# Kernel optimization log

Measured on AMD Instinct MI355X. Metric: run time of the kernel, lower is better.

Reference implementation:

```python
import jax, jax.numpy as jnp
import numpy as np

TEMPERATURE = 30.0
LN_EPS = 1e-5

B, CIN, COUT, S, HID, K = 64, 256, 512, 4096, 64, 4


def setup_inputs() -> dict:
    key = jax.random.key(0)
    ks = jax.random.split(key, 4)
    x = jax.random.normal(ks[0], (B, CIN, S), dtype=jnp.float32)
    w1 = jax.random.normal(ks[1], (HID, CIN), dtype=jnp.float32) * (1.0 / np.sqrt(CIN))
    w2 = jax.random.normal(ks[2], (K, HID), dtype=jnp.float32) * (1.0 / np.sqrt(HID))
    b2 = jnp.zeros((K,), dtype=jnp.float32)
    conv_w = jax.random.normal(ks[3], (K, COUT, CIN), dtype=jnp.float32) * (1.0 / np.sqrt(CIN))
    conv_b = jnp.zeros((K, COUT), dtype=jnp.float32)
    gamma = jnp.ones((S,), dtype=jnp.float32)
    beta = jnp.zeros((S,), dtype=jnp.float32)
    return {"x": x, "w1": w1, "w2": w2, "b2": b2, "conv_w": conv_w,
            "conv_b": conv_b, "gamma": gamma, "beta": beta}


def reference(x, w1, w2, b2, conv_w, conv_b, gamma, beta):
    # --- attention over K kernel experts (global avg pool -> FC -> ReLU -> FC -> softmax/T) ---
    pooled = x.mean(axis=-1)                               # [B, Cin]
    h = jax.nn.relu(pooled @ w1.T)                         # [B, H]
    logits = h @ w2.T + b2                                 # [B, K]
    att = jax.nn.softmax(logits / TEMPERATURE, axis=-1)    # [B, K]
    # --- per-sample mixed 1x1 conv weights (grouped-conv trick == batched matmul) ---
    Wb = jnp.einsum('bk,koi->boi', att, conv_w)            # [B, Cout, Cin]
    bb = att @ conv_b                                      # [B, Cout]
    y = jnp.einsum('boi,bis->bos', Wb, x) + bb[:, :, None]  # [B, Cout, S]
    # --- LayerNorm over time axis (Samples) ---
    mu = y.mean(axis=-1, keepdims=True)
    var = y.var(axis=-1, keepdims=True)
    y = (y - mu) * jax.lax.rsqrt(var + LN_EPS) * gamma + beta
    # --- GELU (torch default: exact erf); dropout is identity in eval mode ---
    return jax.nn.gelu(y, approximate=False)
```

## Files before the change

### kernel.cpp

```cpp
#include <hip/hip_runtime.h>
#include <hip/hip_bf16.h>

#define B_   64
#define CIN  256
#define COUT 512
#define S_   4096
#define HID  64
#define KEXP 4

typedef float f32x4 __attribute__((ext_vector_type(4)));
typedef short bf16x8 __attribute__((ext_vector_type(8)));

static __device__ __forceinline__ unsigned short f2bf(float f) {
    union { float f; unsigned u; } c; c.f = f;
    unsigned r = c.u + 0x7FFFu + ((c.u >> 16) & 1u);
    return (unsigned short)(r >> 16);
}
static __device__ __forceinline__ float bf2f(unsigned short u) {
    union { unsigned u; float f; } c; c.u = ((unsigned)u) << 16;
    return c.f;
}

static __device__ __forceinline__ void gl16(const unsigned short* g, unsigned short* l) {
    __builtin_amdgcn_global_load_lds(
        (const __attribute__((address_space(1))) void*)g,
        (__attribute__((address_space(3))) void*)l,
        16, 0, 0);
}

#define GSTR 68
__global__ __launch_bounds__(512, 2) void k_gram_part(const float* __restrict__ x,
                                                      unsigned short* __restrict__ part,
                                                      float* __restrict__ ppart,
                                                      unsigned short* __restrict__ xF) {
    __shared__ unsigned short lds[256 * GSTR];
    int bid = blockIdx.x;
    int b = bid & 63, sc = bid >> 6;
    int t = threadIdx.x, lane = t & 63, wv = t >> 6;
    int wr = wv >> 1, wc = wv & 1;
    const float* xb = x + (size_t)b * CIN * S_;
    unsigned short* xFb = xF + (size_t)b * S_ * CIN;

    f32x4 acc[4][8] = {};
    float psum[8] = {0.f, 0.f, 0.f, 0.f, 0.f, 0.f, 0.f, 0.f};

    for (int step = 0; step < 16; ++step) {
        int s0 = sc * 1024 + step * 64;
        __syncthreads();
#pragma unroll
        for (int p = 0; p < 8; ++p) {
            int i = t + p * 512;
            int row = i >> 4, f4 = i & 15;
            float4 v = *(const float4*)(xb + (size_t)row * S_ + s0 + f4 * 4);
            psum[p] += v.x + v.y + v.z + v.w;
            unsigned short u[4] = {f2bf(v.x), f2bf(v.y), f2bf(v.z), f2bf(v.w)};
            *(uint2*)&lds[row * GSTR + f4 * 4] = *(const uint2*)u;
        }
        __syncthreads();
        {
#pragma unroll
            for (int it = 0; it < 4; ++it) {
                int slot = t + it * 512;
                int chunk = slot >> 6;
                int st_l = chunk >> 3, kb = chunk & 7;
                int l = slot & 63;
                unsigned short tmp[8];
#pragma unroll
                for (int j = 0; j < 8; ++j)
                    tmp[j] = lds[(kb * 32 + (l >> 4) * 8 + j) * GSTR + st_l * 16 + (l & 15)];
                *(uint4*)(xFb + ((size_t)((s0 >> 4) + st_l) * 8 + kb) * 512 + l * 8) = *(const uint4*)tmp;
            }
        }
#pragma unroll
        for (int kk = 0; kk < 2; ++kk) {
            bf16x8 bfr[8];
#pragma unroll
            for (int nf = 0; nf < 8; ++nf)
                bfr[nf] = *(const bf16x8*)&lds[(wc * 128 + nf * 16 + (lane & 15)) * GSTR + kk * 32 + (lane >> 4) * 8];
#pragma unroll
            for (int mfi = 0; mfi < 4; ++mfi) {
                bf16x8 afr = *(const bf16x8*)&lds[(wr * 64 + mfi * 16 + (lane & 15)) * GSTR + kk * 32 + (lane >> 4) * 8];
#pragma unroll
                for (int nf = 0; nf < 8; ++nf)
                    acc[mfi][nf] = __builtin_amdgcn_mfma_f32_16x16x32_bf16(afr, bfr[nf], acc[mfi][nf], 0, 0, 0);
            }
        }
    }
#pragma unroll
    for (int p = 0; p < 8; ++p) {
        float s = psum[p];
        s += __shfl_xor(s, 1); s += __shfl_xor(s, 2);
        s += __shfl_xor(s, 4); s += __shfl_xor(s, 8);
        if ((t & 15) == 0) ppart[((size_t)sc * 64 + b) * 256 + ((t + p * 512) >> 4)] = s;
    }
    unsigned short* pb = part + ((size_t)sc * 64 + b) * 65536;
#pragma unroll
    for (int mfi = 0; mfi < 4; ++mfi) {
#pragma unroll
        for (int r = 0; r < 4; ++r) {
            int row = wr * 64 + mfi * 16 + (lane >> 4) * 4 + r;
#pragma unroll
            for (int nf = 0; nf < 8; ++nf)
                pb[row * 256 + wc * 128 + nf * 16 + (lane & 15)] = f2bf(acc[mfi][nf][r]);
        }
    }
}

__global__ __launch_bounds__(256) void k_gred(const unsigned short* __restrict__ part,
                                              const float* __restrict__ ppart,
                                              unsigned short* __restrict__ ghat,
                                              float* __restrict__ pooled) {
    int b = blockIdx.x, t = threadIdx.x;
    const size_t bo = (size_t)b * 65536;
    const size_t scs = (size_t)64 * 65536;
    const float inv = 1.f / S_;
    for (int it = 0; it < 32; ++it) {
        size_t i = bo + (size_t)(it * 256 + t) * 8;
        union { uint4 v; unsigned short s[8]; } a0, a1, a2, a3, o;
        a0.v = *(const uint4*)(part + i);
        a1.v = *(const uint4*)(part + scs + i);
        a2.v = *(const uint4*)(part + 2 * scs + i);
        a3.v = *(const uint4*)(part + 3 * scs + i);
#pragma unroll
        for (int j = 0; j < 8; ++j)
            o.s[j] = f2bf((bf2f(a0.s[j]) + bf2f(a1.s[j]) + bf2f(a2.s[j]) + bf2f(a3.s[j])) * inv);
        *(uint4*)&ghat[i] = o.v;
    }
    float p = ppart[(size_t)b * 256 + t] + ppart[(size_t)(64 + b) * 256 + t]
            + ppart[(size_t)(128 + b) * 256 + t] + ppart[(size_t)(192 + b) * 256 + t];
    pooled[b * 256 + t] = p * inv;
}

__global__ __launch_bounds__(64) void k_att(const float* __restrict__ pooled,
                                            const float* __restrict__ w1,
                                            const float* __restrict__ w2,
                                            const float* __restrict__ b2,
                                            float* __restrict__ att_out) {
    int b = blockIdx.x, t = threadIdx.x;
    __shared__ float pl[CIN];
    __shared__ float hl[HID];
    __shared__ float satt[KEXP];
    for (int j = t; j < CIN; j += 64) pl[j] = pooled[b * CIN + j];
    __syncthreads();
    float acc = 0.f;
    const float* w1r = w1 + t * CIN;
#pragma unroll 4
    for (int c = 0; c < CIN; c += 4) {
        float4 w = *(const float4*)(w1r + c);
        acc += w.x * pl[c] + w.y * pl[c + 1] + w.z * pl[c + 2] + w.w * pl[c + 3];
    }
    hl[t] = fmaxf(acc, 0.f);
    __syncthreads();
    if (t < KEXP) {
        float a = 0.f;
        for (int j = 0; j < HID; ++j) a += hl[j] * w2[t * HID + j];
        satt[t] = (a + b2[t]) * (1.0f / 30.0f);
    }
    __syncthreads();
    if (t == 0) {
        float m = fmaxf(fmaxf(satt[0], satt[1]), fmaxf(satt[2], satt[3]));
        float e0 = expf(satt[0] - m), e1 = expf(satt[1] - m);
        float e2 = expf(satt[2] - m), e3 = expf(satt[3] - m);
        float inv = 1.f / (e0 + e1 + e2 + e3);
        att_out[b * KEXP + 0] = e0 * inv;
        att_out[b * KEXP + 1] = e1 * inv;
        att_out[b * KEXP + 2] = e2 * inv;
        att_out[b * KEXP + 3] = e3 * inv;
    }
}

__global__ __launch_bounds__(256) void k_wb(const float* __restrict__ conv_w,
                                            const float* __restrict__ att,
                                            unsigned short* __restrict__ wb) {
    int bid = blockIdx.x;
    int b = bid >> 5, o0 = (bid & 31) * 16;
    int t = threadIdx.x;
    int o = o0 + (t >> 4);
    int i0 = (t & 15) * 16;
    float ak[KEXP];
#pragma unroll
    for (int k = 0; k < KEXP; ++k) ak[k] = att[b * KEXP + k];
    float acc[16];
#pragma unroll
    for (int j = 0; j < 16; ++j) acc[j] = 0.f;
#pragma unroll
    for (int k = 0; k < KEXP; ++k) {
        const float* src = conv_w + ((size_t)(k * COUT + o)) * CIN + i0;
#pragma unroll
        for (int j4 = 0; j4 < 4; ++j4) {
            float4 v = *(const float4*)(src + j4 * 4);
            acc[j4 * 4 + 0] += ak[k] * v.x;
            acc[j4 * 4 + 1] += ak[k] * v.y;
            acc[j4 * 4 + 2] += ak[k] * v.z;
            acc[j4 * 4 + 3] += ak[k] * v.w;
        }
    }
    unsigned short us[16];
#pragma unroll
    for (int j = 0; j < 16; ++j) us[j] = f2bf(acc[j]);
    unsigned short* dst = wb + (size_t)(b * COUT + o) * CIN + i0;
    *(uint4*)(dst) = *(const uint4*)(us);
    *(uint4*)(dst + 8) = *(const uint4*)(us + 8);
}

#define ASTR 264

__global__ __launch_bounds__(256, 2) void k_z(const unsigned short* __restrict__ wb,
                                              const unsigned short* __restrict__ ghat,
                                              float* __restrict__ zout) {
    __shared__ unsigned short lds_a[128 * ASTR];
    int bid = blockIdx.x;
    int b = bid & 63;
    int tile = bid >> 6;
    int m0 = (tile & 3) * 128, n0 = (tile >> 2) * 128;
    int t = threadIdx.x;
    {
        int row = t >> 1, half = t & 1;
        const unsigned short* src = wb + (size_t)(b * COUT + m0 + row) * CIN + half * 128;
        unsigned short* dstrow = &lds_a[row * ASTR + half * 128];
#pragma unroll
        for (int j = 0; j < 16; ++j)
            *(uint4*)(dstrow + j * 8) = *(const uint4*)(src + j * 8);
    }
    __syncthreads();

    int lane = t & 63;
    int wid = t >> 6;
    int arow = lane & 15;
    int kq = lane >> 4;
    int col0 = n0 + wid * 32 + (lane & 15);
    int col1 = col0 + 16;
    const unsigned short* gb = ghat + (size_t)b * 256 * 256;

    f32x4 acc[8][2] = {};
#pragma unroll
    for (int kk = 0; kk < 8; ++kk) {
        bf16x8 b0 = *(const bf16x8*)(gb + (size_t)col0 * 256 + kk * 32 + kq * 8);
        bf16x8 b1 = *(const bf16x8*)(gb + (size_t)col1 * 256 + kk * 32 + kq * 8);
#pragma unroll
        for (int mf = 0; mf < 8; ++mf) {
            int row = mf * 16 + arow;
            bf16x8 a = *(const bf16x8*)&lds_a[row * ASTR + kk * 32 + kq * 8];
            acc[mf][0] = __builtin_amdgcn_mfma_f32_16x16x32_bf16(a, b0, acc[mf][0], 0, 0, 0);
            acc[mf][1] = __builtin_amdgcn_mfma_f32_16x16x32_bf16(a, b1, acc[mf][1], 0, 0, 0);
        }
    }
#pragma unroll
    for (int mf = 0; mf < 8; ++mf) {
#pragma unroll
        for (int r = 0; r < 4; ++r) {
            int row = m0 + mf * 16 + (lane >> 4) * 4 + r;
            size_t rb = ((size_t)b * COUT + row) * 256;
#pragma unroll
            for (int nf = 0; nf < 2; ++nf) {
                int col = n0 + wid * 32 + nf * 16 + (lane & 15);
                zout[rb + col] = acc[mf][nf][r];
            }
        }
    }
}

__global__ __launch_bounds__(256) void k_v(const float* __restrict__ z,
                                           const unsigned short* __restrict__ wb,
                                           const float* __restrict__ pooled,
                                           float* __restrict__ mu,
                                           float* __restrict__ rstd) {
    int gid = blockIdx.x * 4 + (threadIdx.x >> 6);
    int lane = threadIdx.x & 63;
    int b = gid >> 9;
    const float* zr = z + (size_t)gid * 256;
    const unsigned short* wr = wb + (size_t)gid * 256;

    float4 zv = *(const float4*)(zr + lane * 4);
    ushort4 wu = *(const ushort4*)(wr + lane * 4);
    float w0 = bf2f(wu.x), w1 = bf2f(wu.y), w2 = bf2f(wu.z), w3 = bf2f(wu.w);
    float4 pv = *(const float4*)(pooled + b * CIN + lane * 4);

    float v = zv.x * w0 + zv.y * w1 + zv.z * w2 + zv.w * w3;
    float m = pv.x * w0 + pv.y * w1 + pv.z * w2 + pv.w * w3;
#pragma unroll
    for (int off = 1; off < 64; off <<= 1) {
        v += __shfl_xor(v, off);
        m += __shfl_xor(m, off);
    }
    if (lane == 0) {
        float var = v - m * m;
        mu[gid] = m;
        rstd[gid] = rsqrtf(var + 1e-5f);
    }
}

static __device__ __forceinline__ float gelu_t(float z) {
    float d = -1.5957691216f * z * (1.f + 0.044715f * z * z);
    return z * __builtin_amdgcn_rcpf(1.f + __expf(d));
}

#define EPW 66
__global__ __launch_bounds__(512) void k_main14(const unsigned short* __restrict__ xF,
                                                const unsigned short* __restrict__ wb,
                                                const float* __restrict__ mu,
                                                const float* __restrict__ rstd,
                                                const float* __restrict__ gamma,
                                                const float* __restrict__ beta,
                                                float* __restrict__ out) {
    __shared__ unsigned short ring[3][8192];
    __shared__ float eps[8][32 * EPW];
    __shared__ float gb_lds[2048];
    __shared__ float be_lds[2048];

    int bid = blockIdx.x;
    int xcd = bid & 7;
    int local = bid >> 3;
    int rh = local & 1;
    int sq = (local >> 1) & 1;
    int bq = local >> 2;
    int b = xcd + 8 * bq;

    int t = threadIdx.x, lane = t & 63, w = t >> 6;
    int lm = lane & 15, lk = lane >> 4;
    int row0 = rh * 256 + w * 32;
    int colbase = sq * 2048;

    {
        float4 g4 = *(const float4*)(gamma + colbase + t * 4);
        float4 b4 = *(const float4*)(beta + colbase + t * 4);
        *(float4*)&gb_lds[t * 4] = g4;
        *(float4*)&be_lds[t * 4] = b4;
    }

    bf16x8 A[2][8];
    const unsigned short* wbb = wb + (size_t)(b * COUT + row0 + lm) * CIN + lk * 8;
#pragma unroll
    for (int rf = 0; rf < 2; ++rf)
#pragma unroll
        for (int kk = 0; kk < 8; ++kk)
            A[rf][kk] = *(const bf16x8*)(wbb + (size_t)(rf * 16) * CIN + kk * 32);

    int r0 = lane >> 3;
    int c4 = (lane & 7) * 4;
    float muf[4], rsf[4];
#pragma unroll
    for (int j = 0; j < 4; ++j) {
        int row = b * COUT + row0 + r0 + 8 * j;
        muf[j] = mu[row];
        rsf[j] = rstd[row];
    }
    float* outb = out + (size_t)(b * COUT + row0) * S_ + colbase;
    float* epw = &eps[w][0];

    const unsigned short* xFq = xF + (size_t)b * S_ * CIN + (size_t)sq * 524288;

#define STAGE(st_, slot_)                                                          \
    {                                                                              \
        gl16(xFq + (size_t)((st_) * 16 + 2 * w) * 512 + lane * 8,                  \
             &ring[slot_][(2 * w) * 512]);                                         \
        gl16(xFq + (size_t)((st_) * 16 + 2 * w + 1) * 512 + lane * 8,              \
             &ring[slot_][(2 * w + 1) * 512]);                                     \
    }

    STAGE(0, 0)
    STAGE(1, 1)
    __syncthreads();

    for (int st = 0; st < 64; ++st) {
        if (st + 2 < 64) {
            int sp = st + 2, slot = sp - (sp / 3) * 3;
            STAGE(sp, slot)
        }

        const unsigned short* sl = &ring[st - (st / 3) * 3][0];
        f32x4 acc[2][2] = {};
#pragma unroll
        for (int cf = 0; cf < 2; ++cf) {
            bf16x8 Bf[8];
#pragma unroll
            for (int kb = 0; kb < 8; ++kb)
                Bf[kb] = *(const bf16x8*)(sl + (cf * 8 + kb) * 512 + lane * 8);
#pragma unroll
            for (int kb = 0; kb < 8; ++kb) {
                acc[0][cf] = __builtin_amdgcn_mfma_f32_16x16x32_bf16(A[0][kb], Bf[kb], acc[0][cf], 0, 0, 0);
                acc[1][cf] = __builtin_amdgcn_mfma_f32_16x16x32_bf16(A[1][kb], Bf[kb], acc[1][cf], 0, 0, 0);
            }
        }

#pragma unroll
        for (int cf = 0; cf < 2; ++cf)
#pragma unroll
            for (int rf = 0; rf < 2; ++rf)
#pragma unroll
                for (int rr = 0; rr < 4; ++rr)
                    epw[(rf * 16 + lk * 4 + rr) * EPW + (st & 1) * 32 + cf * 16 + lm] =
                        acc[rf][cf][rr];

        if (st & 1) {
            int fg = st >> 1;
#pragma unroll
            for (int j = 0; j < 4; ++j) {
                int rloc = r0 + 8 * j;
#pragma unroll
                for (int seg = 0; seg < 2; ++seg) {
                    int cl = seg * 32 + c4;
                    float2 lo = *(const float2*)&epw[rloc * EPW + cl];
                    float2 hi = *(const float2*)&epw[rloc * EPW + cl + 2];
                    float4 g4 = *(const float4*)&gb_lds[fg * 64 + cl];
                    float4 b4 = *(const float4*)&be_lds[fg * 64 + cl];
                    float4 o;
                    o.x = gelu_t((lo.x - muf[j]) * rsf[j] * g4.x + b4.x);
                    o.y = gelu_t((lo.y - muf[j]) * rsf[j] * g4.y + b4.y);
                    o.z = gelu_t((hi.x - muf[j]) * rsf[j] * g4.z + b4.z);
                    o.w = gelu_t((hi.y - muf[j]) * rsf[j] * g4.w + b4.w);
                    *(float4*)(outb + (size_t)rloc * S_ + fg * 64 + cl) = o;
                }
            }
        }
        __syncthreads();
    }
#undef STAGE
}

extern "C" void kernel_launch(void* const* d_in, const int* in_sizes, int n_in,
                              void* d_out, int out_size, void* d_ws, size_t ws_size,
                              hipStream_t stream) {
    const float* x      = (const float*)d_in[0];
    const float* w1     = (const float*)d_in[1];
    const float* w2     = (const float*)d_in[2];
    const float* b2     = (const float*)d_in[3];
    const float* conv_w = (const float*)d_in[4];
    const float* gamma  = (const float*)d_in[6];
    const float* beta   = (const float*)d_in[7];
    float* out = (float*)d_out;

    float* pooled = (float*)d_ws;
    float* att    = (float*)((char*)d_ws + 65536);
    unsigned short* wb   = (unsigned short*)((char*)d_ws + 262144);
    unsigned short* ghat = (unsigned short*)((char*)d_ws + 17039360);
    float* mu   = (float*)((char*)d_ws + 25427968);
    float* rstd = (float*)((char*)d_ws + 25559040);
    float* ppart = (float*)((char*)d_ws + 25690112);
    unsigned short* xF = (unsigned short*)((char*)d_ws + 33554432);

    unsigned short* part = (unsigned short*)out;
    float* zbuf = (float*)((char*)d_out + 67108864);

    k_gram_part<<<256, 512, 0, stream>>>(x, part, ppart, xF);
    k_gred<<<B_, 256, 0, stream>>>(part, ppart, ghat, pooled);
    k_att<<<B_, 64, 0, stream>>>(pooled, w1, w2, b2, att);
    k_wb<<<B_ * 32, 256, 0, stream>>>(conv_w, att, wb);
    k_z<<<512, 256, 0, stream>>>(wb, ghat, zbuf);
    k_v<<<B_ * COUT / 4, 256, 0, stream>>>(zbuf, wb, pooled, mu, rstd);
    k_main14<<<256, 512, 0, stream>>>(xF, wb, mu, rstd, gamma, beta, out);
}
```

Measured before the change: 438.1 us.

## Halve per-block column span and deepen LDS ring to raise occupancy

The main fused GEMM+LayerNorm+GELU kernel now splits the time axis into four quarters instead of two, launching 512 blocks instead of 256. Each stage loads 16 columns per warp instead of 32 through a 4-deep ring instead of a 3-deep one, which shrinks LDS use. Launch bounds now request 4 blocks per CU, aiming for more resident waves and better latency hiding. The cost is twice as many blocks reloading the same A weights and mu/rstd, plus smaller MFMA batches and more barriers per unit of work.

```diff
diff --git a/kernel.cpp b/kernel.cpp
--- a/kernel.cpp
+++ b/kernel.cpp
@@ -295,37 +295,37 @@
     return z * __builtin_amdgcn_rcpf(1.f + __expf(d));
 }
 
-#define EPW 66
-__global__ __launch_bounds__(512) void k_main14(const unsigned short* __restrict__ xF,
-                                                const unsigned short* __restrict__ wb,
-                                                const float* __restrict__ mu,
-                                                const float* __restrict__ rstd,
-                                                const float* __restrict__ gamma,
-                                                const float* __restrict__ beta,
-                                                float* __restrict__ out) {
-    __shared__ unsigned short ring[3][8192];
+#define EPW 36
+__global__ __launch_bounds__(512, 4) void k_main15(const unsigned short* __restrict__ xF,
+                                                   const unsigned short* __restrict__ wb,
+                                                   const float* __restrict__ mu,
+                                                   const float* __restrict__ rstd,
+                                                   const float* __restrict__ gamma,
+                                                   const float* __restrict__ beta,
+                                                   float* __restrict__ out) {
+    __shared__ unsigned short ring[4][4096];
     __shared__ float eps[8][32 * EPW];
-    __shared__ float gb_lds[2048];
-    __shared__ float be_lds[2048];
+    __shared__ float gb_lds[1024];
+    __shared__ float be_lds[1024];
 
     int bid = blockIdx.x;
     int xcd = bid & 7;
     int local = bid >> 3;
     int rh = local & 1;
-    int sq = (local >> 1) & 1;
-    int bq = local >> 2;
+    int sq = (local >> 1) & 3;
+    int bq = local >> 3;
     int b = xcd + 8 * bq;
 
     int t = threadIdx.x, lane = t & 63, w = t >> 6;
     int lm = lane & 15, lk = lane >> 4;
     int row0 = rh * 256 + w * 32;
-    int colbase = sq * 2048;
+    int colbase = sq * 1024;
 
     {
-        float4 g4 = *(const float4*)(gamma + colbase + t * 4);
-        float4 b4 = *(const float4*)(beta + colbase + t * 4);
-        *(float4*)&gb_lds[t * 4] = g4;
-        *(float4*)&be_lds[t * 4] = b4;
+        float2 g2 = *(const float2*)(gamma + colbase + t * 2);
+        float2 b2v = *(const float2*)(beta + colbase + t * 2);
+        *(float2*)&gb_lds[t * 2] = g2;
+        *(float2*)&be_lds[t * 2] = b2v;
     }
 
     bf16x8 A[2][8];
@@ -348,69 +348,55 @@
     float* outb = out + (size_t)(b * COUT + row0) * S_ + colbase;
     float* epw = &eps[w][0];
 
-    const unsigned short* xFq = xF + (size_t)b * S_ * CIN + (size_t)sq * 524288;
+    const unsigned short* xFq = xF + (size_t)b * S_ * CIN + (size_t)sq * 262144;
 
 #define STAGE(st_, slot_)                                                          \
-    {                                                                              \
-        gl16(xFq + (size_t)((st_) * 16 + 2 * w) * 512 + lane * 8,                  \
-             &ring[slot_][(2 * w) * 512]);                                         \
-        gl16(xFq + (size_t)((st_) * 16 + 2 * w + 1) * 512 + lane * 8,              \
-             &ring[slot_][(2 * w + 1) * 512]);                                     \
-    }
+    gl16(xFq + (size_t)((st_) * 8 + w) * 512 + lane * 8, &ring[slot_][w * 512]);
 
     STAGE(0, 0)
     STAGE(1, 1)
+    STAGE(2, 2)
     __syncthreads();
 
     for (int st = 0; st < 64; ++st) {
-        if (st + 2 < 64) {
-            int sp = st + 2, slot = sp - (sp / 3) * 3;
-            STAGE(sp, slot)
-        }
-
-        const unsigned short* sl = &ring[st - (st / 3) * 3][0];
-        f32x4 acc[2][2] = {};
-#pragma unroll
-        for (int cf = 0; cf < 2; ++cf) {
-            bf16x8 Bf[8];
-#pragma unroll
-            for (int kb = 0; kb < 8; ++kb)
-                Bf[kb] = *(const bf16x8*)(sl + (cf * 8 + kb) * 512 + lane * 8);
-#pragma unroll
-            for (int kb = 0; kb < 8; ++kb) {
-                acc[0][cf] = __builtin_amdgcn_mfma_f32_16x16x32_bf16(A[0][kb], Bf[kb], acc[0][cf], 0, 0, 0);
-                acc[1][cf] = __builtin_amdgcn_mfma_f32_16x16x32_bf16(A[1][kb], Bf[kb], acc[1][cf], 0, 0, 0);
-            }
-        }
-
-#pragma unroll
-        for (int cf = 0; cf < 2; ++cf)
-#pragma unroll
-            for (int rf = 0; rf < 2; ++rf)
-#pragma unroll
-                for (int rr = 0; rr < 4; ++rr)
-                    epw[(rf * 16 + lk * 4 + rr) * EPW + (st & 1) * 32 + cf * 16 + lm] =
-                        acc[rf][cf][rr];
+        if (st + 3 < 64) {
+            int sp = st + 3;
+            STAGE(sp, sp & 3)
+        }
+
+        const unsigned short* sl = &ring[st & 3][0];
+        bf16x8 Bf[8];
+#pragma unroll
+        for (int kb = 0; kb < 8; ++kb)
+            Bf[kb] = *(const bf16x8*)(sl + kb * 512 + lane * 8);
+
+        f32x4 acc[2] = {};
+#pragma unroll
+        for (int kb = 0; kb < 8; ++kb) {
+            acc[0] = __builtin_amdgcn_mfma_f32_16x16x32_bf16(A[0][kb], Bf[kb], acc[0], 0, 0, 0);
+            acc[1] = __builtin_amdgcn_mfma_f32_16x16x32_bf16(A[1][kb], Bf[kb], acc[1], 0, 0, 0);
+        }
+
+#pragma unroll
+        for (int rf = 0; rf < 2; ++rf)
+#pragma unroll
+            for (int rr = 0; rr < 4; ++rr)
+                epw[(rf * 16 + lk * 4 + rr) * EPW + (st & 1) * 16 + lm] = acc[rf][rr];
 
         if (st & 1) {
             int fg = st >> 1;
 #pragma unroll
             for (int j = 0; j < 4; ++j) {
                 int rloc = r0 + 8 * j;
-#pragma unroll
-                for (int seg = 0; seg < 2; ++seg) {
-                    int cl = seg * 32 + c4;
-                    float2 lo = *(const float2*)&epw[rloc * EPW + cl];
-                    float2 hi = *(const float2*)&epw[rloc * EPW + cl + 2];
-                    float4 g4 = *(const float4*)&gb_lds[fg * 64 + cl];
-                    float4 b4 = *(const float4*)&be_lds[fg * 64 + cl];
-                    float4 o;
-                    o.x = gelu_t((lo.x - muf[j]) * rsf[j] * g4.x + b4.x);
-                    o.y = gelu_t((lo.y - muf[j]) * rsf[j] * g4.y + b4.y);
-                    o.z = gelu_t((hi.x - muf[j]) * rsf[j] * g4.z + b4.z);
-                    o.w = gelu_t((hi.y - muf[j]) * rsf[j] * g4.w + b4.w);
-                    *(float4*)(outb + (size_t)rloc * S_ + fg * 64 + cl) = o;
-                }
+                float4 v = *(const float4*)&epw[rloc * EPW + c4];
+                float4 g4 = *(const float4*)&gb_lds[fg * 32 + c4];
+                float4 b4 = *(const float4*)&be_lds[fg * 32 + c4];
+                float4 o;
+                o.x = gelu_t((v.x - muf[j]) * rsf[j] * g4.x + b4.x);
+                o.y = gelu_t((v.y - muf[j]) * rsf[j] * g4.y + b4.y);
+                o.z = gelu_t((v.z - muf[j]) * rsf[j] * g4.z + b4.z);
+                o.w = gelu_t((v.w - muf[j]) * rsf[j] * g4.w + b4.w);
+                *(float4*)(outb + (size_t)rloc * S_ + fg * 32 + c4) = o;
             }
         }
         __syncthreads();
@@ -448,5 +434,5 @@
     k_wb<<<B_ * 32, 256, 0, stream>>>(conv_w, att, wb);
     k_z<<<512, 256, 0, stream>>>(wb, ghat, zbuf);
     k_v<<<B_ * COUT / 4, 256, 0, stream>>>(zbuf, wb, pooled, mu, rstd);
-    k_main14<<<256, 512, 0, stream>>>(xF, wb, mu, rstd, gamma, beta, out);
-}
+    k_main15<<<512, 512, 0, stream>>>(xF, wb, mu, rstd, gamma, beta, out);
+}
```

New measurement: 429.8 us. About the same (-1.9%).
